# Kernel optimization log

Measured on AMD Instinct MI355X. Metric: run time of the kernel, lower is better.

Reference implementation:

```python
import jax, jax.numpy as jnp
import numpy as np

C = 64
CK = C // 8  # query/key channels


def setup_inputs() -> dict:
    key = jax.random.key(0)
    ks = jax.random.split(key, 8)
    b, c, h, w = 4, C, 64, 64
    x = jax.random.normal(ks[0], (b, c, h, w), dtype=jnp.float32)
    # 1x1 conv weights (spectral-normalized weights are still just dense weights at eval)
    wq = jax.random.normal(ks[1], (CK, c), dtype=jnp.float32) * 0.05
    bq = jax.random.normal(ks[2], (CK,), dtype=jnp.float32) * 0.01
    wk = jax.random.normal(ks[3], (CK, c), dtype=jnp.float32) * 0.05
    bk = jax.random.normal(ks[4], (CK,), dtype=jnp.float32) * 0.01
    wv = jax.random.normal(ks[5], (c, c), dtype=jnp.float32) * 0.05
    bv = jax.random.normal(ks[6], (c,), dtype=jnp.float32) * 0.01
    # gamma is initialized to 0 in the module; use a nonzero value so the
    # attention path contributes to the output.
    gamma = jax.random.normal(ks[7], (1,), dtype=jnp.float32) * 0.5
    return {"x": x, "wq": wq, "bq": bq, "wk": wk, "bk": bk,
            "wv": wv, "bv": bv, "gamma": gamma}


def reference(x, wq, bq, wk, bk, wv, bv, gamma):
    b, c, h, w = x.shape
    n = h * w
    xf = x.reshape(b, c, n)                      # [b, c, n]
    # 1x1 convs as matmuls over the channel dim
    q = jnp.einsum('oc,bcn->bno', wq, xf) + bq   # [b, n, ck]
    k = jnp.einsum('oc,bcn->bon', wk, xf) + bk[None, :, None]  # [b, ck, n]
    v = jnp.einsum('oc,bcn->bno', wv, xf) + bv   # [b, n, c]
    attn = jax.nn.softmax(jnp.einsum('bnd,bdm->bnm', q, k), axis=-1)  # [b, n, n]
    o = jnp.einsum('bnm,bmc->bnc', attn, v)      # [b, n, c]
    o = o.transpose(0, 2, 1).reshape(b, c, h, w)
    return gamma[0] * o + x
```

## Files before the change

### kernel.cpp

```cpp
#include <hip/hip_runtime.h>

#define CH 64
#define NN 4096
#define NB 4
#define SPLIT 8
#define KLEN (NN / SPLIT)
#define VSTRIDE 520
#define LOG2E 1.44269504f

typedef unsigned short u16;
typedef unsigned int u32;
typedef __attribute__((ext_vector_type(8))) short bf16x8;
typedef __attribute__((ext_vector_type(16))) float f32x16;

static __device__ __forceinline__ u16 bf16r(float f) {
  union { float f; unsigned u; } v; v.f = f;
  unsigned x = v.u;
  x += 0x7fffu + ((x >> 16) & 1u);
  return (u16)(x >> 16);
}
static __device__ __forceinline__ u32 pk2(float a, float b) {
  union { float f; unsigned u; } va, vb; va.f = a; vb.f = b;
  unsigned x = va.u, y = vb.u;
  x += 0x7fffu + ((x >> 16) & 1u);
  y += 0x7fffu + ((y >> 16) & 1u);
  return (x >> 16) | (y & 0xffff0000u);
}

__global__ __launch_bounds__(192) void qkv_proj(
    const float* __restrict__ x,
    const float* __restrict__ wq, const float* __restrict__ bq,
    const float* __restrict__ wk, const float* __restrict__ bk,
    const float* __restrict__ wv, const float* __restrict__ bv,
    u16* __restrict__ Qb, u16* __restrict__ Kb, u16* __restrict__ Vb) {
  __shared__ float xs[64 * 32];
  __shared__ u16 afr_lds[3][4][64][8];
  const int tid = threadIdx.x;
  const int b = blockIdx.x >> 7;
  const int n0 = (blockIdx.x & 127) << 5;

  for (int i = tid; i < 64 * 32; i += 192)
    xs[i] = x[(size_t)b * CH * NN + (size_t)(i >> 5) * NN + n0 + (i & 31)];
  for (int i = tid; i < 768; i += 192) {
    const int l = i & 63;
    const int s = (i >> 6) & 3;
    const int t = i >> 8;
    const int row = 32 * t + (l & 31);
    const int c0 = 16 * s + 8 * (l >> 5);
    float e[8];
#pragma unroll
    for (int j = 0; j < 8; ++j) {
      float v = 0.f;
      if (row < 64)      v = wv[row * 64 + c0 + j];
      else if (row < 72) v = wq[(row - 64) * 64 + c0 + j];
      else if (row < 80) v = wk[(row - 72) * 64 + c0 + j];
      e[j] = v;
    }
    u32* dst = reinterpret_cast<u32*>(&afr_lds[t][s][l][0]);
    dst[0] = pk2(e[0], e[1]); dst[1] = pk2(e[2], e[3]);
    dst[2] = pk2(e[4], e[5]); dst[3] = pk2(e[6], e[7]);
  }
  __syncthreads();

  const int w = __builtin_amdgcn_readfirstlane(tid >> 6);
  const int lane = tid & 63;
  const int l31 = lane & 31;
  const int h = lane >> 5;
  const int n = n0 + l31;

  f32x16 acc = {};
#pragma unroll
  for (int s = 0; s < 4; ++s) {
    float xv[8];
#pragma unroll
    for (int j = 0; j < 8; ++j)
      xv[j] = xs[(16 * s + 8 * h + j) * 32 + l31];
    union { uint4 u; bf16x8 v; } bf;
    bf.u.x = pk2(xv[0], xv[1]); bf.u.y = pk2(xv[2], xv[3]);
    bf.u.z = pk2(xv[4], xv[5]); bf.u.w = pk2(xv[6], xv[7]);
    const bf16x8 af = *reinterpret_cast<const bf16x8*>(&afr_lds[w][s][lane][0]);
    acc = __builtin_amdgcn_mfma_f32_32x32x16_bf16(af, bf.v, acc, 0, 0, 0);
  }

  if (w < 2) {
    const int sperm = (l31 & 19) | ((l31 & 4) << 1) | ((l31 & 8) >> 1);
    const int nperm = n0 + sperm;
#pragma unroll
    for (int r = 0; r < 16; ++r) {
      const int row = 32 * w + (r & 3) + 8 * (r >> 2) + 4 * h;
      Vb[((size_t)b * CH + row) * NN + nperm] = bf16r(acc[r] + bv[row]);
    }
  } else {
#pragma unroll
    for (int r = 0; r < 8; ++r) {
      const int row = (r & 3) + 8 * (r >> 2) + 4 * h;
      const float v = acc[r];
      if (row < 8)
        Qb[((size_t)b * NN + n) * 8 + row] = bf16r((v + bq[row]) * LOG2E);
      else
        Kb[((size_t)b * NN + n) * 8 + (row - 8)] = bf16r(v + bk[row - 8]);
    }
  }
}

__global__ __launch_bounds__(1024, 4) void flash_attn(
    const u16* __restrict__ Qb, const u16* __restrict__ Kb,
    const u16* __restrict__ Vb, u32* __restrict__ ACCu,
    float* __restrict__ Lb) {
  __shared__ u16 Klds[KLEN * 8 + 8];
  __shared__ u16 Vlds[64 * VSTRIDE];
  const int bid = blockIdx.x;
  const int sp = bid & 7;
  const int rest = bid >> 3;
  const int qc = rest & 7;
  const int b = rest >> 3;
  const int w = __builtin_amdgcn_readfirstlane(threadIdx.x >> 6);
  const int lane = threadIdx.x & 63;
  const int l31 = lane & 31;
  const int h = lane >> 5;
  const int qrow0 = qc * 512 + w * 32;
  const int ks = sp * KLEN;

  if (threadIdx.x < 8) Klds[KLEN * 8 + threadIdx.x] = 0;

  bf16x8 qf = {0, 0, 0, 0, 0, 0, 0, 0};
  if (h == 0)
    qf = *reinterpret_cast<const bf16x8*>(Qb + ((size_t)b * NN + qrow0 + l31) * 8);

  const u16* Kp = Kb + ((size_t)b * NN + ks) * 8;
  const u16* Vp = Vb + (size_t)b * CH * NN + ks;

#pragma unroll
  for (int i = 0; i < 4; ++i) {
    const int ch = 4 * w + i;
    const int m = (ch ^ (ch >> 3)) & 7;
    const u16* src = Vp + (size_t)ch * NN + (((lane & 56) | ((lane ^ m) & 7)) << 3);
    __builtin_amdgcn_global_load_lds(
        (const __attribute__((address_space(1))) void*)src,
        (__attribute__((address_space(3))) void*)&Vlds[ch * VSTRIDE], 16, 0, 0);
  }
  if (w < 8)
    __builtin_amdgcn_global_load_lds(
        (const __attribute__((address_space(1))) void*)(Kp + ((size_t)(64 * w + lane)) * 8),
        (__attribute__((address_space(3))) void*)&Klds[64 * w * 8], 16, 0, 0);
  __syncthreads();

  f32x16 acc0 = {}, acc1 = {};
  const f32x16 zz = {};
  float lsum = 0.f;
  const int m0 = (l31 ^ (l31 >> 3)) & 7;
  const int m1 = m0 ^ 4;

#pragma unroll 4
  for (int kk = 0; kk < KLEN / 32; ++kk) {
    const int kaddr = h ? KLEN * 8 : (kk * 32 + l31) * 8;
    bf16x8 kf = *reinterpret_cast<const bf16x8*>(Klds + kaddr);
    f32x16 s = __builtin_amdgcn_mfma_f32_32x32x16_bf16(kf, qf, zz, 0, 0, 0);
    float p[16];
#pragma unroll
    for (int r = 0; r < 16; ++r) { p[r] = exp2f(s[r]); lsum += p[r]; }
    union { uint4 u; bf16x8 v; } pb0, pb1;
    pb0.u.x = pk2(p[0], p[1]);   pb0.u.y = pk2(p[2], p[3]);
    pb0.u.z = pk2(p[4], p[5]);   pb0.u.w = pk2(p[6], p[7]);
    pb1.u.x = pk2(p[8], p[9]);   pb1.u.y = pk2(p[10], p[11]);
    pb1.u.z = pk2(p[12], p[13]); pb1.u.w = pk2(p[14], p[15]);
    const int g0 = kk * 4 + h;
    const int g1 = g0 + 2;
    const int cp00 = (g0 & 56) | ((g0 ^ m0) & 7);
    const int cp01 = (g1 & 56) | ((g1 ^ m0) & 7);
    const int cp10 = (g0 & 56) | ((g0 ^ m1) & 7);
    const int cp11 = (g1 & 56) | ((g1 ^ m1) & 7);
    bf16x8 v00 = *reinterpret_cast<const bf16x8*>(Vlds + l31 * VSTRIDE + cp00 * 8);
    bf16x8 v01 = *reinterpret_cast<const bf16x8*>(Vlds + l31 * VSTRIDE + cp01 * 8);
    bf16x8 v10 = *reinterpret_cast<const bf16x8*>(Vlds + (32 + l31) * VSTRIDE + cp10 * 8);
    bf16x8 v11 = *reinterpret_cast<const bf16x8*>(Vlds + (32 + l31) * VSTRIDE + cp11 * 8);
    acc0 = __builtin_amdgcn_mfma_f32_32x32x16_bf16(v00, pb0.v, acc0, 0, 0, 0);
    acc0 = __builtin_amdgcn_mfma_f32_32x32x16_bf16(v01, pb1.v, acc0, 0, 0, 0);
    acc1 = __builtin_amdgcn_mfma_f32_32x32x16_bf16(v10, pb0.v, acc1, 0, 0, 0);
    acc1 = __builtin_amdgcn_mfma_f32_32x32x16_bf16(v11, pb1.v, acc1, 0, 0, 0);
  }

  lsum += __shfl_xor(lsum, 32);

  const int gtile = b * (NN / 32) + qc * 16 + w;
  u32* A = ACCu + ((size_t)gtile * SPLIT + sp) * 32 * 32;
#pragma unroll
  for (int rp = 0; rp < 8; ++rp) {
    const int chp = (rp & 1) + 4 * (rp >> 1) + 2 * h;
    __builtin_nontemporal_store(pk2(acc0[2 * rp], acc0[2 * rp + 1]),
                                &A[chp * 32 + l31]);
    __builtin_nontemporal_store(pk2(acc1[2 * rp], acc1[2 * rp + 1]),
                                &A[(16 + chp) * 32 + l31]);
  }
  if (h == 0)
    __builtin_nontemporal_store(lsum, &Lb[((size_t)gtile * SPLIT + sp) * 32 + l31]);
}

__global__ __launch_bounds__(256) void combine(
    const float* __restrict__ x, const float* __restrict__ gamma,
    const u32* __restrict__ ACCu, const float* __restrict__ Lb,
    float* __restrict__ out) {
  const int idx = blockIdx.x * 256 + threadIdx.x;
  const int n4 = idx & (NN / 4 - 1);
  const int cp = (idx >> 10) & 31;
  const int b = idx >> 15;
  const int n = n4 << 2;
  const int gtile = b * (NN / 32) + (n >> 5);
  const int q0 = n & 31;
  const uint4* A4 = reinterpret_cast<const uint4*>(ACCu);
  const float4* L4 = reinterpret_cast<const float4*>(Lb);
  float s0[4] = {0.f, 0.f, 0.f, 0.f}, s1[4] = {0.f, 0.f, 0.f, 0.f};
  float l[4] = {0.f, 0.f, 0.f, 0.f};
#pragma unroll
  for (int sp = 0; sp < SPLIT; ++sp) {
    const uint4 a = A4[(((size_t)gtile * SPLIT + sp) * 32 + cp) * 8 + (q0 >> 2)];
    const float4 lv = L4[(((size_t)gtile * SPLIT + sp) * 32 + q0) >> 2];
    const u32 av[4] = {a.x, a.y, a.z, a.w};
#pragma unroll
    for (int k = 0; k < 4; ++k) {
      union { u32 u; float f; } lo, hi;
      lo.u = av[k] << 16; hi.u = av[k] & 0xffff0000u;
      s0[k] += lo.f; s1[k] += hi.f;
    }
    l[0] += lv.x; l[1] += lv.y; l[2] += lv.z; l[3] += lv.w;
  }
  const float gm = gamma[0];
  float inv[4];
#pragma unroll
  for (int k = 0; k < 4; ++k) inv[k] = gm / l[k];
  const size_t i0 = ((size_t)b * CH + 2 * cp) * NN + n;
  const float4 x0 = *reinterpret_cast<const float4*>(x + i0);
  const float4 x1 = *reinterpret_cast<const float4*>(x + i0 + NN);
  float4 o0, o1;
  o0.x = fmaf(inv[0], s0[0], x0.x); o0.y = fmaf(inv[1], s0[1], x0.y);
  o0.z = fmaf(inv[2], s0[2], x0.z); o0.w = fmaf(inv[3], s0[3], x0.w);
  o1.x = fmaf(inv[0], s1[0], x1.x); o1.y = fmaf(inv[1], s1[1], x1.y);
  o1.z = fmaf(inv[2], s1[2], x1.z); o1.w = fmaf(inv[3], s1[3], x1.w);
  *reinterpret_cast<float4*>(out + i0) = o0;
  *reinterpret_cast<float4*>(out + i0 + NN) = o1;
}

extern "C" void kernel_launch(void* const* d_in, const int* in_sizes, int n_in,
                              void* d_out, int out_size, void* d_ws, size_t ws_size,
                              hipStream_t stream) {
  const float* x     = (const float*)d_in[0];
  const float* wq    = (const float*)d_in[1];
  const float* bq    = (const float*)d_in[2];
  const float* wk    = (const float*)d_in[3];
  const float* bk    = (const float*)d_in[4];
  const float* wv    = (const float*)d_in[5];
  const float* bv    = (const float*)d_in[6];
  const float* gamma = (const float*)d_in[7];
  float* out = (float*)d_out;

  u16* Qb = (u16*)d_ws;
  u16* Kb = Qb + (size_t)NB * NN * 8;
  u16* Vb = Kb + (size_t)NB * NN * 8;
  u32* ACCu = (u32*)(Vb + (size_t)NB * CH * NN);
  float* Lb = (float*)(ACCu + (size_t)NB * (NN / 32) * SPLIT * 32 * 32);

  qkv_proj<<<dim3(NB * (NN / 32)), dim3(192), 0, stream>>>(
      x, wq, bq, wk, bk, wv, bv, Qb, Kb, Vb);
  flash_attn<<<dim3(NB * 8 * SPLIT), dim3(1024), 0, stream>>>(
      Qb, Kb, Vb, ACCu, Lb);
  combine<<<dim3((NB * 32 * (NN / 4)) / 256), dim3(256), 0, stream>>>(
      x, gamma, ACCu, Lb, out);
}
```

Measured before the change: 115.4 us.

## Hoist weight packing, vectorize projection I/O, MFMA row-sums, hardware bf16 packs

Moves the bf16 weight-fragment packing out of every qkv_proj block into a single prep kernel, and vectorizes the x tile load and the Q/K stores. In flash_attn the softmax denominator is now accumulated with an extra MFMA against a ones fragment instead of 16 scalar adds per iteration. Manual bf16 rounding is replaced with the HIP packed float2-to-bf162 conversion. This adds a kernel launch and two more MFMAs per loop iteration in exchange for fewer VALU ops. The row sum is now built from bf16-rounded probabilities rather than fp32 values.

Measured after the change: 115.6 us. Within noise of the previous version (+0.2%).

```diff
diff --git a/kernel.cpp b/kernel.cpp
--- a/kernel.cpp
+++ b/kernel.cpp
@@ -1,4 +1,5 @@
 #include <hip/hip_runtime.h>
+#include <hip/hip_bf16.h>
 
 #define CH 64
 #define NN 4096
@@ -19,32 +20,19 @@
   x += 0x7fffu + ((x >> 16) & 1u);
   return (u16)(x >> 16);
 }
-static __device__ __forceinline__ u32 pk2(float a, float b) {
-  union { float f; unsigned u; } va, vb; va.f = a; vb.f = b;
-  unsigned x = va.u, y = vb.u;
-  x += 0x7fffu + ((x >> 16) & 1u);
-  y += 0x7fffu + ((y >> 16) & 1u);
-  return (x >> 16) | (y & 0xffff0000u);
-}
-
-__global__ __launch_bounds__(192) void qkv_proj(
-    const float* __restrict__ x,
-    const float* __restrict__ wq, const float* __restrict__ bq,
-    const float* __restrict__ wk, const float* __restrict__ bk,
-    const float* __restrict__ wv, const float* __restrict__ bv,
-    u16* __restrict__ Qb, u16* __restrict__ Kb, u16* __restrict__ Vb) {
-  __shared__ float xs[64 * 32];
-  __shared__ u16 afr_lds[3][4][64][8];
-  const int tid = threadIdx.x;
-  const int b = blockIdx.x >> 7;
-  const int n0 = (blockIdx.x & 127) << 5;
-
-  for (int i = tid; i < 64 * 32; i += 192)
-    xs[i] = x[(size_t)b * CH * NN + (size_t)(i >> 5) * NN + n0 + (i & 31)];
-  for (int i = tid; i < 768; i += 192) {
-    const int l = i & 63;
-    const int s = (i >> 6) & 3;
-    const int t = i >> 8;
+static __device__ __forceinline__ u32 pkc(float a, float b) {
+  union { __hip_bfloat162 h; u32 u; } r;
+  r.h = __float22bfloat162_rn(float2{a, b});
+  return r.u;
+}
+
+__global__ __launch_bounds__(192) void prep_w(
+    const float* __restrict__ wq, const float* __restrict__ wk,
+    const float* __restrict__ wv, u16* __restrict__ Afr) {
+  for (int idx = threadIdx.x; idx < 768; idx += 192) {
+    const int l = idx & 63;
+    const int s = (idx >> 6) & 3;
+    const int t = idx >> 8;
     const int row = 32 * t + (l & 31);
     const int c0 = 16 * s + 8 * (l >> 5);
     float e[8];
@@ -56,9 +44,27 @@
       else if (row < 80) v = wk[(row - 72) * 64 + c0 + j];
       e[j] = v;
     }
-    u32* dst = reinterpret_cast<u32*>(&afr_lds[t][s][l][0]);
-    dst[0] = pk2(e[0], e[1]); dst[1] = pk2(e[2], e[3]);
-    dst[2] = pk2(e[4], e[5]); dst[3] = pk2(e[6], e[7]);
+    u32* dst = reinterpret_cast<u32*>(Afr + (size_t)idx * 8);
+    dst[0] = pkc(e[0], e[1]); dst[1] = pkc(e[2], e[3]);
+    dst[2] = pkc(e[4], e[5]); dst[3] = pkc(e[6], e[7]);
+  }
+}
+
+__global__ __launch_bounds__(192) void qkv_proj(
+    const float* __restrict__ x, const u16* __restrict__ Afr,
+    const float* __restrict__ bq, const float* __restrict__ bk,
+    const float* __restrict__ bv,
+    u16* __restrict__ Qb, u16* __restrict__ Kb, u16* __restrict__ Vb) {
+  __shared__ float xs[64 * 32];
+  const int tid = threadIdx.x;
+  const int b = blockIdx.x >> 7;
+  const int n0 = (blockIdx.x & 127) << 5;
+
+  const float* xbase = x + (size_t)b * CH * NN + n0;
+  for (int i = tid; i < 512; i += 192) {
+    const int row = i >> 3, c4 = i & 7;
+    *reinterpret_cast<float4*>(&xs[row * 32 + c4 * 4]) =
+        *reinterpret_cast<const float4*>(xbase + (size_t)row * NN + c4 * 4);
   }
   __syncthreads();
 
@@ -71,14 +77,15 @@
   f32x16 acc = {};
 #pragma unroll
   for (int s = 0; s < 4; ++s) {
+    const bf16x8 af = *reinterpret_cast<const bf16x8*>(
+        Afr + ((size_t)(w * 4 + s) * 64 + lane) * 8);
     float xv[8];
 #pragma unroll
     for (int j = 0; j < 8; ++j)
       xv[j] = xs[(16 * s + 8 * h + j) * 32 + l31];
     union { uint4 u; bf16x8 v; } bf;
-    bf.u.x = pk2(xv[0], xv[1]); bf.u.y = pk2(xv[2], xv[3]);
-    bf.u.z = pk2(xv[4], xv[5]); bf.u.w = pk2(xv[6], xv[7]);
-    const bf16x8 af = *reinterpret_cast<const bf16x8*>(&afr_lds[w][s][lane][0]);
+    bf.u.x = pkc(xv[0], xv[1]); bf.u.y = pkc(xv[2], xv[3]);
+    bf.u.z = pkc(xv[4], xv[5]); bf.u.w = pkc(xv[6], xv[7]);
     acc = __builtin_amdgcn_mfma_f32_32x32x16_bf16(af, bf.v, acc, 0, 0, 0);
   }
 
@@ -91,15 +98,19 @@
       Vb[((size_t)b * CH + row) * NN + nperm] = bf16r(acc[r] + bv[row]);
     }
   } else {
-#pragma unroll
-    for (int r = 0; r < 8; ++r) {
-      const int row = (r & 3) + 8 * (r >> 2) + 4 * h;
-      const float v = acc[r];
-      if (row < 8)
-        Qb[((size_t)b * NN + n) * 8 + row] = bf16r((v + bq[row]) * LOG2E);
-      else
-        Kb[((size_t)b * NN + n) * 8 + (row - 8)] = bf16r(v + bk[row - 8]);
-    }
+    const float q0 = (acc[0] + bq[4 * h + 0]) * LOG2E;
+    const float q1 = (acc[1] + bq[4 * h + 1]) * LOG2E;
+    const float q2 = (acc[2] + bq[4 * h + 2]) * LOG2E;
+    const float q3 = (acc[3] + bq[4 * h + 3]) * LOG2E;
+    const float k0 = acc[4] + bk[4 * h + 0];
+    const float k1 = acc[5] + bk[4 * h + 1];
+    const float k2 = acc[6] + bk[4 * h + 2];
+    const float k3 = acc[7] + bk[4 * h + 3];
+    uint2 qv, kv;
+    qv.x = pkc(q0, q1); qv.y = pkc(q2, q3);
+    kv.x = pkc(k0, k1); kv.y = pkc(k2, k3);
+    *reinterpret_cast<uint2*>(Qb + ((size_t)b * NN + n) * 8 + 4 * h) = qv;
+    *reinterpret_cast<uint2*>(Kb + ((size_t)b * NN + n) * 8 + 4 * h) = kv;
   }
 }
 
@@ -145,9 +156,12 @@
         (__attribute__((address_space(3))) void*)&Klds[64 * w * 8], 16, 0, 0);
   __syncthreads();
 
-  f32x16 acc0 = {}, acc1 = {};
+  f32x16 acc0 = {}, acc1 = {}, acc2 = {};
   const f32x16 zz = {};
-  float lsum = 0.f;
+  const short one = (short)0x3F80;
+  const bf16x8 zero8 = {0, 0, 0, 0, 0, 0, 0, 0};
+  const bf16x8 ones8 = {one, one, one, one, one, one, one, one};
+  const bf16x8 af1 = (l31 == 0) ? ones8 : zero8;
   const int m0 = (l31 ^ (l31 >> 3)) & 7;
   const int m1 = m0 ^ 4;
 
@@ -158,12 +172,12 @@
     f32x16 s = __builtin_amdgcn_mfma_f32_32x32x16_bf16(kf, qf, zz, 0, 0, 0);
     float p[16];
 #pragma unroll
-    for (int r = 0; r < 16; ++r) { p[r] = exp2f(s[r]); lsum += p[r]; }
+    for (int r = 0; r < 16; ++r) p[r] = exp2f(s[r]);
     union { uint4 u; bf16x8 v; } pb0, pb1;
-    pb0.u.x = pk2(p[0], p[1]);   pb0.u.y = pk2(p[2], p[3]);
-    pb0.u.z = pk2(p[4], p[5]);   pb0.u.w = pk2(p[6], p[7]);
-    pb1.u.x = pk2(p[8], p[9]);   pb1.u.y = pk2(p[10], p[11]);
-    pb1.u.z = pk2(p[12], p[13]); pb1.u.w = pk2(p[14], p[15]);
+    pb0.u.x = pkc(p[0], p[1]);   pb0.u.y = pkc(p[2], p[3]);
+    pb0.u.z = pkc(p[4], p[5]);   pb0.u.w = pkc(p[6], p[7]);
+    pb1.u.x = pkc(p[8], p[9]);   pb1.u.y = pkc(p[10], p[11]);
+    pb1.u.z = pkc(p[12], p[13]); pb1.u.w = pkc(p[14], p[15]);
     const int g0 = kk * 4 + h;
     const int g1 = g0 + 2;
     const int cp00 = (g0 & 56) | ((g0 ^ m0) & 7);
@@ -178,8 +192,11 @@
     acc0 = __builtin_amdgcn_mfma_f32_32x32x16_bf16(v01, pb1.v, acc0, 0, 0, 0);
     acc1 = __builtin_amdgcn_mfma_f32_32x32x16_bf16(v10, pb0.v, acc1, 0, 0, 0);
     acc1 = __builtin_amdgcn_mfma_f32_32x32x16_bf16(v11, pb1.v, acc1, 0, 0, 0);
-  }
-
+    acc2 = __builtin_amdgcn_mfma_f32_32x32x16_bf16(af1, pb0.v, acc2, 0, 0, 0);
+    acc2 = __builtin_amdgcn_mfma_f32_32x32x16_bf16(af1, pb1.v, acc2, 0, 0, 0);
+  }
+
+  float lsum = acc2[0];
   lsum += __shfl_xor(lsum, 32);
 
   const int gtile = b * (NN / 32) + qc * 16 + w;
@@ -187,9 +204,9 @@
 #pragma unroll
   for (int rp = 0; rp < 8; ++rp) {
     const int chp = (rp & 1) + 4 * (rp >> 1) + 2 * h;
-    __builtin_nontemporal_store(pk2(acc0[2 * rp], acc0[2 * rp + 1]),
+    __builtin_nontemporal_store(pkc(acc0[2 * rp], acc0[2 * rp + 1]),
                                 &A[chp * 32 + l31]);
-    __builtin_nontemporal_store(pk2(acc1[2 * rp], acc1[2 * rp + 1]),
+    __builtin_nontemporal_store(pkc(acc1[2 * rp], acc1[2 * rp + 1]),
                                 &A[(16 + chp) * 32 + l31]);
   }
   if (h == 0)
@@ -258,9 +275,11 @@
   u16* Vb = Kb + (size_t)NB * NN * 8;
   u32* ACCu = (u32*)(Vb + (size_t)NB * CH * NN);
   float* Lb = (float*)(ACCu + (size_t)NB * (NN / 32) * SPLIT * 32 * 32);
-
+  u16* Afr = (u16*)(Lb + (size_t)NB * (NN / 32) * SPLIT * 32);
+
+  prep_w<<<dim3(1), dim3(192), 0, stream>>>(wq, wk, wv, Afr);
   qkv_proj<<<dim3(NB * (NN / 32)), dim3(192), 0, stream>>>(
-      x, wq, bq, wk, bk, wv, bv, Qb, Kb, Vb);
+      x, Afr, bq, bk, bv, Qb, Kb, Vb);
   flash_attn<<<dim3(NB * 8 * SPLIT), dim3(1024), 0, stream>>>(
       Qb, Kb, Vb, ACCu, Lb);
   combine<<<dim3((NB * 32 * (NN / 4)) / 256), dim3(256), 0, stream>>>(
```
